# Kernel tuning notes

Hardware: AMD Instinct MI355X
Metric: run time of the kernel (lower is better)

## Reference

```python
import jax, jax.numpy as jnp
import numpy as np

EMBED_DIM = 768
N_HEADS = 12
HEAD_SIZE = EMBED_DIM // N_HEADS


def setup_inputs() -> dict:
    key = jax.random.key(0)
    k1, k2, k3, k4 = jax.random.split(key, 4)
    B, T, C = 512, 128, EMBED_DIM
    x = jax.random.normal(k1, (B, T, C), dtype=jnp.float32)
    # torch Linear weights: [out, in]
    w_qkv = jax.random.normal(k2, (3 * C, C), dtype=jnp.float32) / np.sqrt(C)
    w_proj = jax.random.normal(k3, (C, C), dtype=jnp.float32) / np.sqrt(C)
    b_proj = jax.random.normal(k4, (C,), dtype=jnp.float32) * 0.01
    return {"x": x, "w_qkv": w_qkv, "w_proj": w_proj, "b_proj": b_proj}


def reference(x, w_qkv, w_proj, b_proj):
    B, T, C = x.shape
    H, D = N_HEADS, HEAD_SIZE
    qkv = jnp.einsum('btc,oc->bto', x, w_qkv)  # [B,T,3C]
    q, k, v = jnp.split(qkv, 3, axis=-1)
    # [B,T,C] -> [B,H,T,D]
    q = q.reshape(B, T, H, D).transpose(0, 2, 1, 3)
    k = k.reshape(B, T, H, D).transpose(0, 2, 1, 3)
    v = v.reshape(B, T, H, D).transpose(0, 2, 1, 3)
    wei = jnp.einsum('bhtd,bhsd->bhts', q, k)  # [B,H,T,T]
    causal = jnp.tril(jnp.ones((T, T), dtype=bool))  # True where allowed
    wei = jnp.where(causal, wei, -jnp.inf)
    # original scales AFTER masking (-inf stays -inf)
    wei = jax.nn.softmax(wei / jnp.sqrt(jnp.asarray(D, x.dtype)), axis=-1)
    out = jnp.einsum('bhts,bhsd->bhtd', wei, v)  # [B,H,T,D]
    out = out.transpose(0, 2, 1, 3).reshape(B, T, C)
    # proj; dropout is identity in eval mode
    out = jnp.einsum('btc,oc->bto', out, w_proj) + b_proj
    return out
```

## Files before the change

### kernel.cpp

```cpp
#include <hip/hip_runtime.h>
#include <hip/hip_bf16.h>

typedef __bf16 bf16_t;
typedef __attribute__((ext_vector_type(8))) __bf16 bf16x8;
typedef __attribute__((ext_vector_type(4))) float f32x4;

#define B_SZ 512
#define T_SZ 128
#define C_SZ 768
#define H_SZ 12
#define D_SZ 64
#define M_SZ (B_SZ * T_SZ)
#define NQKV (3 * C_SZ)

__global__ __launch_bounds__(256) void cvt_f32_bf16(
    const float* __restrict__ in, bf16_t* __restrict__ out, int n)
{
    int i = (blockIdx.x * blockDim.x + threadIdx.x) * 8;
    int stride = gridDim.x * blockDim.x * 8;
    for (; i < n; i += stride) {
        float4 a = *reinterpret_cast<const float4*>(in + i);
        float4 b = *reinterpret_cast<const float4*>(in + i + 4);
        bf16x8 o;
        o[0] = (bf16_t)a.x; o[1] = (bf16_t)a.y;
        o[2] = (bf16_t)a.z; o[3] = (bf16_t)a.w;
        o[4] = (bf16_t)b.x; o[5] = (bf16_t)b.y;
        o[6] = (bf16_t)b.z; o[7] = (bf16_t)b.w;
        *reinterpret_cast<bf16x8*>(out + i) = o;
    }
}

__device__ __forceinline__ void gload16(const bf16_t* g, const char* l)
{
    __builtin_amdgcn_global_load_lds(
        (const __attribute__((address_space(1))) void*)g,
        (__attribute__((address_space(3))) void*)l, 16, 0, 0);
}

#define BAR() do { asm volatile("" ::: "memory"); \
                   __builtin_amdgcn_s_barrier(); \
                   asm volatile("" ::: "memory"); } while (0)

#define LD_A(mh, bb) do { \
    _Pragma("unroll") for (int m_ = 0; m_ < 4; ++m_) { \
        af[m_][0] = *(const bf16x8*)(rdAk0 + (bb)*32768 + ((mh)*64 + m_*16)*128); \
        af[m_][1] = *(const bf16x8*)(rdAk1 + (bb)*32768 + ((mh)*64 + m_*16)*128); } } while (0)

#define LD_B(nh, bb) do { \
    _Pragma("unroll") for (int n_ = 0; n_ < 2; ++n_) { \
        bf[(nh)*2+n_][0] = *(const bf16x8*)(rdBk0 + (bb)*32768 + ((nh)*2+n_)*2048); \
        bf[(nh)*2+n_][1] = *(const bf16x8*)(rdBk1 + (bb)*32768 + ((nh)*2+n_)*2048); } } while (0)

#define ST_A(bb, hf, u) do { if ((u) < nt) { \
    const bf16_t* s_ = pA + (size_t)((hf)*128) * K + (size_t)(u)*64; \
    char* d_ = ldsAw + (bb)*32768 + (hf)*16384; \
    gload16(s_, d_); gload16(s_ + (size_t)8*K, d_ + 1024); } } while (0)

#define ST_B(bb, hf, u) do { if ((u) < nt) { \
    const bf16_t* s_ = pB + (size_t)((hf)*128) * K + (size_t)(u)*64; \
    char* d_ = ldsBw + (bb)*32768 + (hf)*16384; \
    gload16(s_, d_); gload16(s_ + (size_t)8*K, d_ + 1024); } } while (0)

#define MF_Q(mh, nh) do { __builtin_amdgcn_s_setprio(1); \
    _Pragma("unroll") for (int m_ = 0; m_ < 4; ++m_) \
    _Pragma("unroll") for (int n_ = 0; n_ < 2; ++n_) { \
        acc[(mh)*4+m_][(nh)*2+n_] = __builtin_amdgcn_mfma_f32_16x16x32_bf16( \
            af[m_][0], bf[(nh)*2+n_][0], acc[(mh)*4+m_][(nh)*2+n_], 0, 0, 0); \
        acc[(mh)*4+m_][(nh)*2+n_] = __builtin_amdgcn_mfma_f32_16x16x32_bf16( \
            af[m_][1], bf[(nh)*2+n_][1], acc[(mh)*4+m_][(nh)*2+n_], 0, 0, 0); } \
    __builtin_amdgcn_s_setprio(0); } while (0)

#define VMC(n) asm volatile("s_waitcnt vmcnt(" #n ")" ::: "memory")

template <bool BF16_OUT, bool BIAS>
__global__ __launch_bounds__(512, 2) void gemm256(
    const bf16_t* __restrict__ A, const bf16_t* __restrict__ Bt,
    void* __restrict__ Cout, const float* __restrict__ bias,
    int M, int N, int K, int nx)
{
    __shared__ char smem[131072];

    const int tid  = threadIdx.x;
    const int lane = tid & 63;
    const int w    = tid >> 6;
    const int wr   = w >> 2;
    const int wc   = w & 3;

    const int nwg = gridDim.x;
    int bid = blockIdx.x;
    if ((nwg & 7) == 0) bid = (bid & 7) * (nwg >> 3) + (bid >> 3);
    const int bx = bid % nx;
    const int by = bid / nx;
    const size_t bm = (size_t)by * 256;
    const size_t bn = (size_t)bx * 256;

    const int nt    = K >> 6;
    const int niter = nt >> 1;

    const int i3    = lane >> 3;
    const int colSw = ((lane & 7) ^ i3) * 8;
    const bf16_t* pA = A  + (bm + (size_t)(w * 16 + i3)) * K + colSw;
    const bf16_t* pB = Bt + (bn + (size_t)(w * 16 + i3)) * K + colSw;
    char* ldsAw = smem + w * 2048;
    char* ldsBw = smem + 65536 + w * 2048;

    const int lane_lo = lane & 15;
    const int sxr  = (lane & 7) << 4;
    const int cK0  = (((lane >> 4) * 16) ^ sxr);
    const int cK1  = cK0 ^ 64;
    const char* rdAk0 = smem + wr * 16384 + lane_lo * 128 + cK0;
    const char* rdAk1 = smem + wr * 16384 + lane_lo * 128 + cK1;
    const char* rdBk0 = smem + 65536 + (wc >> 1) * 16384 + ((wc & 1) * 64 + lane_lo) * 128 + cK0;
    const char* rdBk1 = smem + 65536 + (wc >> 1) * 16384 + ((wc & 1) * 64 + lane_lo) * 128 + cK1;

    f32x4  acc[8][4] = {};
    bf16x8 af[4][2];
    bf16x8 bf[4][2];

    ST_A(0, 0, 0); ST_A(0, 1, 0); ST_B(0, 0, 0); ST_B(0, 1, 0);
    ST_B(1, 0, 1); ST_B(1, 1, 1);
    VMC(4);
    BAR();

    for (int it = 0; it < niter; ++it) {
        const int u = it * 2;
        const bool last = (it + 1 == niter);
        LD_A(0, 0); LD_B(0, 0); ST_A(1, 0, u + 1); BAR(); MF_Q(0, 0); BAR();
        LD_B(1, 0);             ST_A(1, 1, u + 1); BAR(); MF_Q(0, 1); BAR();
        LD_A(1, 0);             ST_B(0, 0, u + 2); BAR(); MF_Q(1, 0); BAR();
                                ST_B(0, 1, u + 2); BAR(); MF_Q(1, 1);
        if (last) { VMC(0); } else { VMC(4); }
        BAR();
        LD_A(0, 1); LD_B(0, 1); ST_A(0, 0, u + 2); BAR(); MF_Q(0, 0); BAR();
        LD_B(1, 1);             ST_A(0, 1, u + 2); BAR(); MF_Q(0, 1); BAR();
        LD_A(1, 1);             ST_B(1, 0, u + 3); BAR(); MF_Q(1, 0); BAR();
                                ST_B(1, 1, u + 3); BAR(); MF_Q(1, 1);
        if (last) { VMC(0); } else { VMC(4); }
        BAR();
    }

    const int crow = (lane >> 4) * 4;
    const int ccol = lane & 15;
    #pragma unroll
    for (int n = 0; n < 4; ++n) {
        const size_t col = bn + wc * 64 + n * 16 + ccol;
        float bv = 0.f;
        if constexpr (BIAS) bv = bias[col];
        #pragma unroll
        for (int m = 0; m < 8; ++m) {
            #pragma unroll
            for (int r = 0; r < 4; ++r) {
                const size_t row = bm + wr * 128 + m * 16 + crow + r;
                float v = acc[m][n][r] + bv;
                if constexpr (BF16_OUT)
                    ((bf16_t*)Cout)[row * N + col] = (bf16_t)v;
                else
                    ((float*)Cout)[row * N + col] = v;
            }
        }
    }
}

__global__ __launch_bounds__(256) void attn_kernel(
    const bf16_t* __restrict__ qkv, bf16_t* __restrict__ outp)
{
    __shared__ bf16_t Ks[128 * 64];
    __shared__ bf16_t Vt[64 * 128];
    __shared__ bf16_t Ps[128 * 128];

    const int h    = blockIdx.x;
    const int b    = blockIdx.y;
    const int tid  = threadIdx.x;
    const int lane = tid & 63;
    const int wave = tid >> 6;

    const bf16_t* base = qkv + (size_t)b * T_SZ * NQKV + h * D_SZ;

    #pragma unroll
    for (int p = 0; p < 4; ++p) {
        int e   = p * 256 + tid;
        int row = e >> 3;
        int col = (e & 7) * 8;
        int4 kv = *reinterpret_cast<const int4*>(base + (size_t)row * NQKV + C_SZ + col);
        int kb = row * 128 + ((col * 2) ^ ((row & 7) << 4));
        *reinterpret_cast<int4*>((char*)Ks + kb) = kv;

        bf16x8 vv = *reinterpret_cast<const bf16x8*>(base + (size_t)row * NQKV + 2 * C_SZ + col);
        #pragma unroll
        for (int j = 0; j < 8; ++j) {
            int d  = col + j;
            int vb = d * 256 + ((row * 2) ^ ((d & 7) << 4));
            *reinterpret_cast<bf16_t*>((char*)Vt + vb) = vv[j];
        }
    }

    bf16x8 qf[2][2];
    #pragma unroll
    for (int mi = 0; mi < 2; ++mi)
        #pragma unroll
        for (int ks = 0; ks < 2; ++ks) {
            int m = wave * 32 + mi * 16 + (lane & 15);
            int d = ks * 32 + (lane >> 4) * 8;
            qf[mi][ks] = *reinterpret_cast<const bf16x8*>(base + (size_t)m * NQKV + d);
        }

    __syncthreads();

    f32x4 s[2][8] = {};
    #pragma unroll
    for (int ks = 0; ks < 2; ++ks) {
        int koff = ks * 32 + (lane >> 4) * 8;
        #pragma unroll
        for (int nj = 0; nj < 8; ++nj) {
            int n  = nj * 16 + (lane & 15);
            int kb = n * 128 + ((koff * 2) ^ ((n & 7) << 4));
            bf16x8 kf = *reinterpret_cast<const bf16x8*>((char*)Ks + kb);
            #pragma unroll
            for (int mi = 0; mi < 2; ++mi)
                s[mi][nj] = __builtin_amdgcn_mfma_f32_16x16x32_bf16(
                    qf[mi][ks], kf, s[mi][nj], 0, 0, 0);
        }
    }

    const float scale = 0.125f;
    #pragma unroll
    for (int mi = 0; mi < 2; ++mi) {
        #pragma unroll
        for (int r = 0; r < 4; ++r) {
            int m = wave * 32 + mi * 16 + ((lane >> 4) << 2) + r;
            float sv[8];
            float mx = -3.0e38f;
            #pragma unroll
            for (int nj = 0; nj < 8; ++nj) {
                int n   = nj * 16 + (lane & 15);
                float v = s[mi][nj][r] * scale;
                v = (n <= m) ? v : -3.0e38f;
                sv[nj] = v;
                mx = fmaxf(mx, v);
            }
            #pragma unroll
            for (int off = 1; off < 16; off <<= 1)
                mx = fmaxf(mx, __shfl_xor(mx, off));
            float sum = 0.f;
            #pragma unroll
            for (int nj = 0; nj < 8; ++nj) {
                float p = __expf(sv[nj] - mx);
                sv[nj] = p;
                sum += p;
            }
            #pragma unroll
            for (int off = 1; off < 16; off <<= 1)
                sum += __shfl_xor(sum, off);
            float inv = 1.0f / sum;
            #pragma unroll
            for (int nj = 0; nj < 8; ++nj) {
                int n  = nj * 16 + (lane & 15);
                int pb = m * 256 + ((n * 2) ^ ((m & 7) << 4));
                *reinterpret_cast<bf16_t*>((char*)Ps + pb) = (bf16_t)(sv[nj] * inv);
            }
        }
    }

    __syncthreads();

    f32x4 o[2][4] = {};
    #pragma unroll
    for (int ks = 0; ks < 4; ++ks) {
        int soff = ks * 32 + (lane >> 4) * 8;
        bf16x8 pf[2];
        #pragma unroll
        for (int mi = 0; mi < 2; ++mi) {
            int m  = wave * 32 + mi * 16 + (lane & 15);
            int pb = m * 256 + ((soff * 2) ^ ((m & 7) << 4));
            pf[mi] = *reinterpret_cast<const bf16x8*>((char*)Ps + pb);
        }
        #pragma unroll
        for (int nj = 0; nj < 4; ++nj) {
            int d  = nj * 16 + (lane & 15);
            int vb = d * 256 + ((soff * 2) ^ ((d & 7) << 4));
            bf16x8 vf = *reinterpret_cast<const bf16x8*>((char*)Vt + vb);
            #pragma unroll
            for (int mi = 0; mi < 2; ++mi)
                o[mi][nj] = __builtin_amdgcn_mfma_f32_16x16x32_bf16(
                    pf[mi], vf, o[mi][nj], 0, 0, 0);
        }
    }

    bf16_t* op = outp + (size_t)b * T_SZ * C_SZ + h * D_SZ;
    #pragma unroll
    for (int mi = 0; mi < 2; ++mi) {
        #pragma unroll
        for (int nj = 0; nj < 4; ++nj) {
            #pragma unroll
            for (int r = 0; r < 4; ++r) {
                int m = wave * 32 + mi * 16 + ((lane >> 4) << 2) + r;
                int d = nj * 16 + (lane & 15);
                op[(size_t)m * C_SZ + d] = (bf16_t)o[mi][nj][r];
            }
        }
    }
}

extern "C" void kernel_launch(void* const* d_in, const int* in_sizes, int n_in,
                              void* d_out, int out_size, void* d_ws, size_t ws_size,
                              hipStream_t stream)
{
    const float* x      = (const float*)d_in[0];
    const float* w_qkv  = (const float*)d_in[1];
    const float* w_proj = (const float*)d_in[2];
    const float* b_proj = (const float*)d_in[3];

    const int n_x     = M_SZ * C_SZ;
    const int n_wqkv  = NQKV * C_SZ;
    const int n_wproj = C_SZ * C_SZ;

    char* ws = (char*)d_ws;
    bf16_t* xb     = (bf16_t*)ws;
    bf16_t* wqkvb  = (bf16_t*)(ws + (size_t)n_x * 2);
    bf16_t* wprojb = (bf16_t*)(ws + (size_t)n_x * 2 + (size_t)n_wqkv * 2);
    bf16_t* qkvb   = (bf16_t*)(ws + (size_t)n_x * 2 + (size_t)n_wqkv * 2 + (size_t)n_wproj * 2);
    bf16_t* attnb  = xb;

    cvt_f32_bf16<<<4096, 256, 0, stream>>>(x, xb, n_x);
    cvt_f32_bf16<<<(n_wqkv / 8 + 255) / 256, 256, 0, stream>>>(w_qkv, wqkvb, n_wqkv);
    cvt_f32_bf16<<<(n_wproj / 8 + 255) / 256, 256, 0, stream>>>(w_proj, wprojb, n_wproj);

    gemm256<true, false><<<dim3((NQKV / 256) * (M_SZ / 256)), 512, 0, stream>>>(
        xb, wqkvb, qkvb, nullptr, M_SZ, NQKV, C_SZ, NQKV / 256);

    attn_kernel<<<dim3(H_SZ, B_SZ), 256, 0, stream>>>(qkvb, attnb);

    gemm256<false, true><<<dim3((C_SZ / 256) * (M_SZ / 256)), 512, 0, stream>>>(
        attnb, wprojb, d_out, b_proj, M_SZ, C_SZ, C_SZ, C_SZ / 256);
}
```

Measured before the change: 546.4 us.

## Restructure GEMM main loop to halve barriers and reuse LDS fragments

```diff
diff --git a/kernel.cpp b/kernel.cpp
--- a/kernel.cpp
+++ b/kernel.cpp
@@ -41,15 +41,23 @@
                    __builtin_amdgcn_s_barrier(); \
                    asm volatile("" ::: "memory"); } while (0)
 
-#define LD_A(mh, bb) do { \
-    _Pragma("unroll") for (int m_ = 0; m_ < 4; ++m_) { \
-        af[m_][0] = *(const bf16x8*)(rdAk0 + (bb)*32768 + ((mh)*64 + m_*16)*128); \
-        af[m_][1] = *(const bf16x8*)(rdAk1 + (bb)*32768 + ((mh)*64 + m_*16)*128); } } while (0)
-
-#define LD_B(nh, bb) do { \
-    _Pragma("unroll") for (int n_ = 0; n_ < 2; ++n_) { \
-        bf[(nh)*2+n_][0] = *(const bf16x8*)(rdBk0 + (bb)*32768 + ((nh)*2+n_)*2048); \
-        bf[(nh)*2+n_][1] = *(const bf16x8*)(rdBk1 + (bb)*32768 + ((nh)*2+n_)*2048); } } while (0)
+#define VMC(n) asm volatile("s_waitcnt vmcnt(" #n ")" ::: "memory")
+
+#define RD_A0(bb) do { _Pragma("unroll") for (int m_ = 0; m_ < 4; ++m_) { \
+    af0[m_][0] = *(const bf16x8*)(rdAk0 + (bb)*32768 + m_*2048); \
+    af0[m_][1] = *(const bf16x8*)(rdAk1 + (bb)*32768 + m_*2048); } } while (0)
+
+#define RD_AY(bb) do { _Pragma("unroll") for (int m_ = 0; m_ < 4; ++m_) { \
+    afY[m_][0] = *(const bf16x8*)(rdAk0 + (bb)*32768 + 8192 + m_*2048); \
+    afY[m_][1] = *(const bf16x8*)(rdAk1 + (bb)*32768 + 8192 + m_*2048); } } while (0)
+
+#define RD_B01(bb) do { _Pragma("unroll") for (int n_ = 0; n_ < 2; ++n_) { \
+    b01[n_][0] = *(const bf16x8*)(rdBk0 + (bb)*32768 + n_*2048); \
+    b01[n_][1] = *(const bf16x8*)(rdBk1 + (bb)*32768 + n_*2048); } } while (0)
+
+#define RD_B23(bb) do { _Pragma("unroll") for (int n_ = 0; n_ < 2; ++n_) { \
+    b23[n_][0] = *(const bf16x8*)(rdBk0 + (bb)*32768 + 4096 + n_*2048); \
+    b23[n_][1] = *(const bf16x8*)(rdBk1 + (bb)*32768 + 4096 + n_*2048); } } while (0)
 
 #define ST_A(bb, hf, u) do { if ((u) < nt) { \
     const bf16_t* s_ = pA + (size_t)((hf)*128) * K + (size_t)(u)*64; \
@@ -61,16 +69,14 @@
     char* d_ = ldsBw + (bb)*32768 + (hf)*16384; \
     gload16(s_, d_); gload16(s_ + (size_t)8*K, d_ + 1024); } } while (0)
 
-#define MF_Q(mh, nh) do { __builtin_amdgcn_s_setprio(1); \
+#define MFQ(A_, B_, mo, no) do { __builtin_amdgcn_s_setprio(1); \
     _Pragma("unroll") for (int m_ = 0; m_ < 4; ++m_) \
     _Pragma("unroll") for (int n_ = 0; n_ < 2; ++n_) { \
-        acc[(mh)*4+m_][(nh)*2+n_] = __builtin_amdgcn_mfma_f32_16x16x32_bf16( \
-            af[m_][0], bf[(nh)*2+n_][0], acc[(mh)*4+m_][(nh)*2+n_], 0, 0, 0); \
-        acc[(mh)*4+m_][(nh)*2+n_] = __builtin_amdgcn_mfma_f32_16x16x32_bf16( \
-            af[m_][1], bf[(nh)*2+n_][1], acc[(mh)*4+m_][(nh)*2+n_], 0, 0, 0); } \
+        acc[(mo)+m_][(no)+n_] = __builtin_amdgcn_mfma_f32_16x16x32_bf16( \
+            A_[m_][0], B_[n_][0], acc[(mo)+m_][(no)+n_], 0, 0, 0); \
+        acc[(mo)+m_][(no)+n_] = __builtin_amdgcn_mfma_f32_16x16x32_bf16( \
+            A_[m_][1], B_[n_][1], acc[(mo)+m_][(no)+n_], 0, 0, 0); } \
     __builtin_amdgcn_s_setprio(0); } while (0)
-
-#define VMC(n) asm volatile("s_waitcnt vmcnt(" #n ")" ::: "memory")
 
 template <bool BF16_OUT, bool BIAS>
 __global__ __launch_bounds__(512, 2) void gemm256(
@@ -114,27 +120,26 @@
     const char* rdBk1 = smem + 65536 + (wc >> 1) * 16384 + ((wc & 1) * 64 + lane_lo) * 128 + cK1;
 
     f32x4  acc[8][4] = {};
-    bf16x8 af[4][2];
-    bf16x8 bf[4][2];
-
-    ST_A(0, 0, 0); ST_A(0, 1, 0); ST_B(0, 0, 0); ST_B(0, 1, 0);
-    ST_B(1, 0, 1); ST_B(1, 1, 1);
+    bf16x8 af0[4][2], afY[4][2], b01[2][2], b23[2][2];
+
+    ST_B(0, 0, 0); ST_A(0, 0, 0); ST_A(0, 1, 0); ST_B(0, 1, 0);
+    ST_B(1, 0, 1); ST_A(1, 0, 1);
     VMC(4);
     BAR();
 
     for (int it = 0; it < niter; ++it) {
         const int u = it * 2;
         const bool last = (it + 1 == niter);
-        LD_A(0, 0); LD_B(0, 0); ST_A(1, 0, u + 1); BAR(); MF_Q(0, 0); BAR();
-        LD_B(1, 0);             ST_A(1, 1, u + 1); BAR(); MF_Q(0, 1); BAR();
-        LD_A(1, 0);             ST_B(0, 0, u + 2); BAR(); MF_Q(1, 0); BAR();
-                                ST_B(0, 1, u + 2); BAR(); MF_Q(1, 1);
+        RD_A0(0); RD_B01(0); RD_B23(0); ST_A(1, 1, u + 1); MFQ(af0, b01, 0, 0); BAR();
+        RD_AY(0);                        ST_B(1, 1, u + 1); MFQ(af0, b23, 0, 2); BAR();
+                                         ST_B(0, 0, u + 2); MFQ(afY, b01, 4, 0); BAR();
+                                         ST_A(0, 0, u + 2); MFQ(afY, b23, 4, 2);
         if (last) { VMC(0); } else { VMC(4); }
         BAR();
-        LD_A(0, 1); LD_B(0, 1); ST_A(0, 0, u + 2); BAR(); MF_Q(0, 0); BAR();
-        LD_B(1, 1);             ST_A(0, 1, u + 2); BAR(); MF_Q(0, 1); BAR();
-        LD_A(1, 1);             ST_B(1, 0, u + 3); BAR(); MF_Q(1, 0); BAR();
-                                ST_B(1, 1, u + 3); BAR(); MF_Q(1, 1);
+        RD_A0(1); RD_B01(1); RD_B23(1); ST_A(0, 1, u + 2); MFQ(af0, b01, 0, 0); BAR();
+        RD_AY(1);                        ST_B(0, 1, u + 2); MFQ(af0, b23, 0, 2); BAR();
+                                         ST_B(1, 0, u + 3); MFQ(afY, b01, 4, 0); BAR();
+                                         ST_A(1, 0, u + 3); MFQ(afY, b23, 4, 2);
         if (last) { VMC(0); } else { VMC(4); }
         BAR();
     }
```

Measured after the change: 533.3 us. 1.02x faster.
